# Kernel optimization log

Hardware: AMD Instinct MI355X
Metric: run time of the kernel (lower is better)

The kernel has to match this reference:

```python
import jax, jax.numpy as jnp
import numpy as np


def _logmvv(a, b, c, NT):
    """Log-space batched matrix-vector-vector product (SparseKernelHmmLm.logmvv).

    a: (N, T, C)     log potentials per sparse state
    b: (N, T, C, D)  log left features
    c: (N, T, C, D)  log right features
    Returns (N, T, D, D): out[n,t,i,j] = logsumexp_c(a[n,t,c] + b[n,t,c,i] + c[n,t,c,j])
    Tokens are flattened and zero-padded to NT rows, as in the original kernel.
    """
    N, T, C = a.shape
    D = b.shape[-1]
    nt = N * T
    pad = NT - nt
    af = jnp.concatenate([a.reshape(nt, C), jnp.zeros((pad, C), a.dtype)], 0)          # (NT, C)
    bf = jnp.concatenate([b.reshape(nt, C, D), jnp.zeros((pad, C, D), b.dtype)], 0)    # (NT, C, D)
    cf = jnp.concatenate([c.reshape(nt, C, D), jnp.zeros((pad, C, D), c.dtype)], 0)    # (NT, C, D)

    ab = af[:, :, None] + bf                      # (NT, C, D) log(a*b)
    m1 = jnp.max(ab, axis=1)                      # (NT, D) stabilizer for left factor
    m2 = jnp.max(cf, axis=1)                      # (NT, D) stabilizer for right factor
    e1 = jnp.exp(ab - m1[:, None, :])             # (NT, C, D)
    e2 = jnp.exp(cf - m2[:, None, :])             # (NT, C, D)
    # contraction over sparse states C -> (NT, D, D)
    s = jnp.einsum('nci,ncj->nij', e1, e2)
    out = jnp.log(s) + m1[:, :, None] + m2[:, None, :]
    return out[:nt].reshape(N, T, D, D)


def setup_inputs() -> dict:
    key = jax.random.key(0)
    k1, k2, k3 = jax.random.split(key, 3)
    N, T, C, D = 8, 250, 128, 64
    a = jax.random.normal(k1, (N, T, C), dtype=jnp.float32)
    b = jax.random.normal(k2, (N, T, C, D), dtype=jnp.float32)
    c = jax.random.normal(k3, (N, T, C, D), dtype=jnp.float32)
    return {"a": a, "b": b, "c": c, "NT": 2048}


def reference(a, b, c, NT):
    return _logmvv(a, b, c, NT)
```

## Files before the change

### kernel.cpp

```cpp
#include <hip/hip_runtime.h>
#include <stdint.h>

typedef __attribute__((ext_vector_type(8))) short short8;
typedef __attribute__((ext_vector_type(4))) float f32x4;

#define CDIM 128
#define DDIM 64

__device__ __forceinline__ uint32_t pack2_bf16(float a, float b) {
  uint32_t ua = __float_as_uint(a);
  uint32_t ub = __float_as_uint(b);
  ua = (ua + 0x7FFFu + ((ua >> 16) & 1u)) >> 16;
  ub = (ub + 0x7FFFu + ((ub >> 16) & 1u)) >> 16;
  return ua | (ub << 16);
}

__global__ __launch_bounds__(256, 8) void logmvv_kernel(
    const float* __restrict__ a, const float* __restrict__ b,
    const float* __restrict__ c, float* __restrict__ out) {
  __shared__ float a_lds[CDIM];
  __shared__ __align__(16) uint16_t e2T[DDIM * CDIM];

  const int row = blockIdx.x;
  const int t = threadIdx.x;
  const int lane = t & 63;
  const int w = t >> 6;
  const int l15 = lane & 15;
  const int lq = lane >> 4;
  const int swz = (lane & 7) << 4;

  const float* bp = b + (size_t)row * (CDIM * DDIM);
  const float* cp = c + (size_t)row * (CDIM * DDIM);

  if (t < CDIM) a_lds[t] = a[(size_t)row * CDIM + t];

  char* e2b = (char*)e2T;
#pragma unroll
  for (int k = 0; k < 4; ++k) {
    float cv[8];
#pragma unroll
    for (int p = 0; p < 8; ++p) cv[p] = cp[(w * 32 + k * 8 + p) * DDIM + lane];
    const uint32_t r0 = pack2_bf16(__expf(cv[0]), __expf(cv[1]));
    const uint32_t r1 = pack2_bf16(__expf(cv[2]), __expf(cv[3]));
    const uint32_t r2 = pack2_bf16(__expf(cv[4]), __expf(cv[5]));
    const uint32_t r3 = pack2_bf16(__expf(cv[6]), __expf(cv[7]));
    *(uint4*)(e2b + lane * 256 + ((w * 64 + k * 16) ^ swz)) =
        make_uint4(r0, r1, r2, r3);
  }

  __syncthreads();

  short8 afrag[4];
  const int colA = 16 * w + l15;
#pragma unroll
  for (int kk = 0; kk < 4; ++kk) {
    const int cbase = kk * 32 + lq * 8;
    float bv[8];
#pragma unroll
    for (int e = 0; e < 8; ++e)
      bv[e] = bp[(cbase + e) * DDIM + colA] + a_lds[cbase + e];
    union { uint32_t u[4]; short8 s; } fr;
    fr.u[0] = pack2_bf16(__expf(bv[0]), __expf(bv[1]));
    fr.u[1] = pack2_bf16(__expf(bv[2]), __expf(bv[3]));
    fr.u[2] = pack2_bf16(__expf(bv[4]), __expf(bv[5]));
    fr.u[3] = pack2_bf16(__expf(bv[6]), __expf(bv[7]));
    afrag[kk] = fr.s;
  }

  f32x4 acc[4];
#pragma unroll
  for (int tj = 0; tj < 4; ++tj) acc[tj] = (f32x4){0.f, 0.f, 0.f, 0.f};

#pragma unroll
  for (int kk = 0; kk < 4; ++kk) {
    const int cb = kk * 64 + lq * 16;
#pragma unroll
    for (int tj = 0; tj < 4; ++tj) {
      const short8 bf =
          *(const short8*)(e2b + (16 * tj + l15) * 256 + (cb ^ swz));
      acc[tj] =
          __builtin_amdgcn_mfma_f32_16x16x32_bf16(afrag[kk], bf, acc[tj], 0, 0, 0);
    }
  }

  float* op = out + (size_t)row * (DDIM * DDIM);
#pragma unroll
  for (int tj = 0; tj < 4; ++tj) {
#pragma unroll
    for (int rr = 0; rr < 4; ++rr) {
      op[(16 * w + lq * 4 + rr) * DDIM + 16 * tj + l15] = __logf(acc[tj][rr]);
    }
  }
}

extern "C" void kernel_launch(void* const* d_in, const int* in_sizes, int n_in,
                              void* d_out, int out_size, void* d_ws, size_t ws_size,
                              hipStream_t stream) {
  const float* a = (const float*)d_in[0];
  const float* b = (const float*)d_in[1];
  const float* c = (const float*)d_in[2];
  float* out = (float*)d_out;
  const int nt = in_sizes[0] / CDIM;
  logmvv_kernel<<<nt, 256, 0, stream>>>(a, b, c, out);
}
```

Before: 29.26 us.

## Use one wave per row with register fragments, dropping the LDS transpose

Switches from four waves per token row, which staged exp(c) through swizzled LDS, to a single 64-lane wave per row. That wave loads both b and c fragments straight from global memory into registers and computes the full 64x64 output with a 4x4 grid of MFMA accumulators. This removes the LDS staging, the barrier and the shared a buffer. In exchange each wave needs far more registers (64 accumulator floats plus 64 loaded values per step), has less parallelism per row, and makes strided 16-wide global loads.

```diff
diff --git a/kernel.cpp b/kernel.cpp
--- a/kernel.cpp
+++ b/kernel.cpp
@@ -15,82 +15,80 @@
   return ua | (ub << 16);
 }
 
-__global__ __launch_bounds__(256, 8) void logmvv_kernel(
+__global__ __launch_bounds__(64, 2) void logmvv_kernel(
     const float* __restrict__ a, const float* __restrict__ b,
     const float* __restrict__ c, float* __restrict__ out) {
-  __shared__ float a_lds[CDIM];
-  __shared__ __align__(16) uint16_t e2T[DDIM * CDIM];
-
   const int row = blockIdx.x;
-  const int t = threadIdx.x;
-  const int lane = t & 63;
-  const int w = t >> 6;
+  const int lane = threadIdx.x;
   const int l15 = lane & 15;
   const int lq = lane >> 4;
-  const int swz = (lane & 7) << 4;
 
+  const float* ap = a + (size_t)row * CDIM;
   const float* bp = b + (size_t)row * (CDIM * DDIM);
   const float* cp = c + (size_t)row * (CDIM * DDIM);
 
-  if (t < CDIM) a_lds[t] = a[(size_t)row * CDIM + t];
+  f32x4 acc[4][4];
+#pragma unroll
+  for (int tr = 0; tr < 4; ++tr)
+#pragma unroll
+    for (int tj = 0; tj < 4; ++tj) acc[tr][tj] = (f32x4){0.f, 0.f, 0.f, 0.f};
 
-  char* e2b = (char*)e2T;
-#pragma unroll
-  for (int k = 0; k < 4; ++k) {
-    float cv[8];
-#pragma unroll
-    for (int p = 0; p < 8; ++p) cv[p] = cp[(w * 32 + k * 8 + p) * DDIM + lane];
-    const uint32_t r0 = pack2_bf16(__expf(cv[0]), __expf(cv[1]));
-    const uint32_t r1 = pack2_bf16(__expf(cv[2]), __expf(cv[3]));
-    const uint32_t r2 = pack2_bf16(__expf(cv[4]), __expf(cv[5]));
-    const uint32_t r3 = pack2_bf16(__expf(cv[6]), __expf(cv[7]));
-    *(uint4*)(e2b + lane * 256 + ((w * 64 + k * 16) ^ swz)) =
-        make_uint4(r0, r1, r2, r3);
-  }
-
-  __syncthreads();
-
-  short8 afrag[4];
-  const int colA = 16 * w + l15;
 #pragma unroll
   for (int kk = 0; kk < 4; ++kk) {
     const int cbase = kk * 32 + lq * 8;
-    float bv[8];
+
+    const float4 a0 = *(const float4*)(ap + cbase);
+    const float4 a1 = *(const float4*)(ap + cbase + 4);
+    float bv[4][8], cv[4][8];
 #pragma unroll
-    for (int e = 0; e < 8; ++e)
-      bv[e] = bp[(cbase + e) * DDIM + colA] + a_lds[cbase + e];
-    union { uint32_t u[4]; short8 s; } fr;
-    fr.u[0] = pack2_bf16(__expf(bv[0]), __expf(bv[1]));
-    fr.u[1] = pack2_bf16(__expf(bv[2]), __expf(bv[3]));
-    fr.u[2] = pack2_bf16(__expf(bv[4]), __expf(bv[5]));
-    fr.u[3] = pack2_bf16(__expf(bv[6]), __expf(bv[7]));
-    afrag[kk] = fr.s;
-  }
+    for (int tr = 0; tr < 4; ++tr)
+#pragma unroll
+      for (int e = 0; e < 8; ++e)
+        bv[tr][e] = bp[(cbase + e) * DDIM + 16 * tr + l15];
+#pragma unroll
+    for (int tj = 0; tj < 4; ++tj)
+#pragma unroll
+      for (int e = 0; e < 8; ++e)
+        cv[tj][e] = cp[(cbase + e) * DDIM + 16 * tj + l15];
 
-  f32x4 acc[4];
+    const float av[8] = {a0.x, a0.y, a0.z, a0.w, a1.x, a1.y, a1.z, a1.w};
+
+    short8 afrag[4], bfrag[4];
 #pragma unroll
-  for (int tj = 0; tj < 4; ++tj) acc[tj] = (f32x4){0.f, 0.f, 0.f, 0.f};
+    for (int tr = 0; tr < 4; ++tr) {
+      union { uint32_t u[4]; short8 s; } fr;
+#pragma unroll
+      for (int p = 0; p < 4; ++p)
+        fr.u[p] = pack2_bf16(__expf(av[2 * p] + bv[tr][2 * p]),
+                             __expf(av[2 * p + 1] + bv[tr][2 * p + 1]));
+      afrag[tr] = fr.s;
+    }
+#pragma unroll
+    for (int tj = 0; tj < 4; ++tj) {
+      union { uint32_t u[4]; short8 s; } fr;
+#pragma unroll
+      for (int p = 0; p < 4; ++p)
+        fr.u[p] = pack2_bf16(__expf(cv[tj][2 * p]), __expf(cv[tj][2 * p + 1]));
+      bfrag[tj] = fr.s;
+    }
 
 #pragma unroll
-  for (int kk = 0; kk < 4; ++kk) {
-    const int cb = kk * 64 + lq * 16;
+    for (int tr = 0; tr < 4; ++tr)
 #pragma unroll
-    for (int tj = 0; tj < 4; ++tj) {
-      const short8 bf =
-          *(const short8*)(e2b + (16 * tj + l15) * 256 + (cb ^ swz));
-      acc[tj] =
-          __builtin_amdgcn_mfma_f32_16x16x32_bf16(afrag[kk], bf, acc[tj], 0, 0, 0);
-    }
+      for (int tj = 0; tj < 4; ++tj)
+        acc[tr][tj] = __builtin_amdgcn_mfma_f32_16x16x32_bf16(
+            afrag[tr], bfrag[tj], acc[tr][tj], 0, 0, 0);
   }
 
   float* op = out + (size_t)row * (DDIM * DDIM);
 #pragma unroll
-  for (int tj = 0; tj < 4; ++tj) {
+  for (int tr = 0; tr < 4; ++tr)
 #pragma unroll
-    for (int rr = 0; rr < 4; ++rr) {
-      op[(16 * w + lq * 4 + rr) * DDIM + 16 * tj + l15] = __logf(acc[tj][rr]);
-    }
-  }
+    for (int tj = 0; tj < 4; ++tj)
+#pragma unroll
+      for (int rr = 0; rr < 4; ++rr)
+        op[(16 * tr + lq * 4 + rr) * DDIM + 16 * tj + l15] =
+            __logf(acc[tr][tj][rr]);
 }
 
 extern "C" void kernel_launch(void* const* d_in, const int* in_sizes, int n_in,
@@ -101,5 +99,5 @@
   const float* c = (const float*)d_in[2];
   float* out = (float*)d_out;
   const int nt = in_sizes[0] / CDIM;
-  logmvv_kernel<<<nt, 256, 0, stream>>>(a, b, c, out);
+  logmvv_kernel<<<nt, 64, 0, stream>>>(a, b, c, out);
 }
```

New measurement: 37.27 us. 1.27x slower.

## Issue all global loads up front and drop the a LDS staging

Applied to the files above, without the earlier changes.

All of c, b and a are now loaded into registers at kernel start, so the memory requests overlap instead of being issued in dependent batches. The a vector is read straight from global with float4 loads rather than staged through shared memory. The A-fragment exp/pack work is moved before the barrier so it overlaps the LDS writes of other waves. The extra live registers mean launch bounds drop from 8 to 4 blocks per SIMD hint, which may reduce occupancy.

```diff
diff --git a/kernel.cpp b/kernel.cpp
--- a/kernel.cpp
+++ b/kernel.cpp
@@ -15,10 +15,9 @@
   return ua | (ub << 16);
 }
 
-__global__ __launch_bounds__(256, 8) void logmvv_kernel(
+__global__ __launch_bounds__(256, 4) void logmvv_kernel(
     const float* __restrict__ a, const float* __restrict__ b,
     const float* __restrict__ c, float* __restrict__ out) {
-  __shared__ float a_lds[CDIM];
   __shared__ __align__(16) uint16_t e2T[DDIM * CDIM];
 
   const int row = blockIdx.x;
@@ -29,43 +28,54 @@
   const int lq = lane >> 4;
   const int swz = (lane & 7) << 4;
 
+  const float* ap = a + (size_t)row * CDIM;
   const float* bp = b + (size_t)row * (CDIM * DDIM);
   const float* cp = c + (size_t)row * (CDIM * DDIM);
 
-  if (t < CDIM) a_lds[t] = a[(size_t)row * CDIM + t];
+  float cv[32];
+#pragma unroll
+  for (int p = 0; p < 32; ++p) cv[p] = cp[(w * 32 + p) * DDIM + lane];
+
+  const int colA = 16 * w + l15;
+  float bvv[4][8];
+#pragma unroll
+  for (int kk = 0; kk < 4; ++kk)
+#pragma unroll
+    for (int e = 0; e < 8; ++e)
+      bvv[kk][e] = bp[(kk * 32 + lq * 8 + e) * DDIM + colA];
+  float av[4][8];
+#pragma unroll
+  for (int kk = 0; kk < 4; ++kk) {
+    const float4 a0 = *(const float4*)(ap + kk * 32 + lq * 8);
+    const float4 a1 = *(const float4*)(ap + kk * 32 + lq * 8 + 4);
+    av[kk][0] = a0.x; av[kk][1] = a0.y; av[kk][2] = a0.z; av[kk][3] = a0.w;
+    av[kk][4] = a1.x; av[kk][5] = a1.y; av[kk][6] = a1.z; av[kk][7] = a1.w;
+  }
 
   char* e2b = (char*)e2T;
 #pragma unroll
   for (int k = 0; k < 4; ++k) {
-    float cv[8];
-#pragma unroll
-    for (int p = 0; p < 8; ++p) cv[p] = cp[(w * 32 + k * 8 + p) * DDIM + lane];
-    const uint32_t r0 = pack2_bf16(__expf(cv[0]), __expf(cv[1]));
-    const uint32_t r1 = pack2_bf16(__expf(cv[2]), __expf(cv[3]));
-    const uint32_t r2 = pack2_bf16(__expf(cv[4]), __expf(cv[5]));
-    const uint32_t r3 = pack2_bf16(__expf(cv[6]), __expf(cv[7]));
+    const uint32_t r0 = pack2_bf16(__expf(cv[k * 8 + 0]), __expf(cv[k * 8 + 1]));
+    const uint32_t r1 = pack2_bf16(__expf(cv[k * 8 + 2]), __expf(cv[k * 8 + 3]));
+    const uint32_t r2 = pack2_bf16(__expf(cv[k * 8 + 4]), __expf(cv[k * 8 + 5]));
+    const uint32_t r3 = pack2_bf16(__expf(cv[k * 8 + 6]), __expf(cv[k * 8 + 7]));
     *(uint4*)(e2b + lane * 256 + ((w * 64 + k * 16) ^ swz)) =
         make_uint4(r0, r1, r2, r3);
   }
 
-  __syncthreads();
-
   short8 afrag[4];
-  const int colA = 16 * w + l15;
 #pragma unroll
   for (int kk = 0; kk < 4; ++kk) {
-    const int cbase = kk * 32 + lq * 8;
-    float bv[8];
+    union { uint32_t u[4]; short8 s; } fr;
 #pragma unroll
-    for (int e = 0; e < 8; ++e)
-      bv[e] = bp[(cbase + e) * DDIM + colA] + a_lds[cbase + e];
-    union { uint32_t u[4]; short8 s; } fr;
-    fr.u[0] = pack2_bf16(__expf(bv[0]), __expf(bv[1]));
-    fr.u[1] = pack2_bf16(__expf(bv[2]), __expf(bv[3]));
-    fr.u[2] = pack2_bf16(__expf(bv[4]), __expf(bv[5]));
-    fr.u[3] = pack2_bf16(__expf(bv[6]), __expf(bv[7]));
+    for (int p = 0; p < 4; ++p)
+      fr.u[p] = pack2_bf16(__expf(av[kk][2 * p] + bvv[kk][2 * p]),
+                           __expf(av[kk][2 * p + 1] + bvv[kk][2 * p + 1]));
     afrag[kk] = fr.s;
   }
+  asm volatile("" ::"v"(afrag[0]), "v"(afrag[1]), "v"(afrag[2]), "v"(afrag[3]));
+
+  __syncthreads();
 
   f32x4 acc[4];
 #pragma unroll
@@ -85,12 +95,10 @@
 
   float* op = out + (size_t)row * (DDIM * DDIM);
 #pragma unroll
-  for (int tj = 0; tj < 4; ++tj) {
+  for (int tj = 0; tj < 4; ++tj)
 #pragma unroll
-    for (int rr = 0; rr < 4; ++rr) {
+    for (int rr = 0; rr < 4; ++rr)
       op[(16 * w + lq * 4 + rr) * DDIM + 16 * tj + l15] = __logf(acc[tj][rr]);
-    }
-  }
 }
 
 extern "C" void kernel_launch(void* const* d_in, const int* in_sizes, int n_in,
```

Measured after the change: 29.28 us. About the same (+0.1%).

## Process eight rows per block with double-buffered async global-to-LDS staging

Applied to the files above, without the earlier changes.

Each block now handles eight token rows in sequence instead of one. The b and c tiles for the next row are prefetched with global_load_lds into a second LDS buffer while the current row is exponentiated and multiplied, with hand-placed vmcnt waits and barriers between the stages. The aim is to hide global memory latency behind compute and to cut per-block launch overhead. The cost is about 148 KB of LDS per block, which allows one block (four waves) per CU and sharply lowers occupancy and memory-level parallelism for this bandwidth-bound kernel.

```diff
diff --git a/kernel.cpp b/kernel.cpp
--- a/kernel.cpp
+++ b/kernel.cpp
@@ -6,6 +6,7 @@
 
 #define CDIM 128
 #define DDIM 64
+#define RPB 8
 
 __device__ __forceinline__ uint32_t pack2_bf16(float a, float b) {
   uint32_t ua = __float_as_uint(a);
@@ -15,82 +16,130 @@
   return ua | (ub << 16);
 }
 
-__global__ __launch_bounds__(256, 8) void logmvv_kernel(
+__global__ __launch_bounds__(256, 1) void logmvv_kernel(
     const float* __restrict__ a, const float* __restrict__ b,
-    const float* __restrict__ c, float* __restrict__ out) {
-  __shared__ float a_lds[CDIM];
+    const float* __restrict__ c, float* __restrict__ out, int nt) {
+  __shared__ __align__(16) float bRaw[2][CDIM * DDIM];
+  __shared__ __align__(16) float cRaw[2][CDIM * DDIM];
   __shared__ __align__(16) uint16_t e2T[DDIM * CDIM];
+  __shared__ __align__(16) float aLds[RPB * CDIM];
 
-  const int row = blockIdx.x;
   const int t = threadIdx.x;
   const int lane = t & 63;
   const int w = t >> 6;
   const int l15 = lane & 15;
   const int lq = lane >> 4;
   const int swz = (lane & 7) << 4;
+  const int bid = blockIdx.x;
+  const int row0 = bid * RPB;
+  const int rows = (nt - row0 < RPB) ? (nt - row0) : RPB;
 
-  const float* bp = b + (size_t)row * (CDIM * DDIM);
-  const float* cp = c + (size_t)row * (CDIM * DDIM);
+  __builtin_amdgcn_global_load_lds(
+      (const __attribute__((address_space(1))) void*)(a + (size_t)row0 * CDIM +
+                                                      w * 256 + lane * 4),
+      (__attribute__((address_space(3))) void*)((char*)aLds + w * 1024), 16, 0, 0);
 
-  if (t < CDIM) a_lds[t] = a[(size_t)row * CDIM + t];
-
-  char* e2b = (char*)e2T;
-#pragma unroll
-  for (int k = 0; k < 4; ++k) {
-    float cv[8];
-#pragma unroll
-    for (int p = 0; p < 8; ++p) cv[p] = cp[(w * 32 + k * 8 + p) * DDIM + lane];
-    const uint32_t r0 = pack2_bf16(__expf(cv[0]), __expf(cv[1]));
-    const uint32_t r1 = pack2_bf16(__expf(cv[2]), __expf(cv[3]));
-    const uint32_t r2 = pack2_bf16(__expf(cv[4]), __expf(cv[5]));
-    const uint32_t r3 = pack2_bf16(__expf(cv[6]), __expf(cv[7]));
-    *(uint4*)(e2b + lane * 256 + ((w * 64 + k * 16) ^ swz)) =
-        make_uint4(r0, r1, r2, r3);
+#define STAGE(ridx, buf)                                                        \
+  {                                                                             \
+    const float* bsrc = b + (size_t)(ridx) * (CDIM * DDIM);                     \
+    const float* csrc = c + (size_t)(ridx) * (CDIM * DDIM);                     \
+    _Pragma("unroll") for (int q = 0; q < 8; ++q) {                             \
+      const int chunk = w * 8 + q;                            \
+      __builtin_amdgcn_global_load_lds(                                         \
+          (const __attribute__((address_space(1))) void*)(bsrc + chunk * 256 +  \
+                                                          lane * 4),            \
+          (__attribute__((address_space(3))) void*)((char*)bRaw[buf] +          \
+                                                    chunk * 1024),              \
+          16, 0, 0);                                                            \
+      __builtin_amdgcn_global_load_lds(                                         \
+          (const __attribute__((address_space(1))) void*)(csrc + chunk * 256 +  \
+                                                          lane * 4),            \
+          (__attribute__((address_space(3))) void*)((char*)cRaw[buf] +          \
+                                                    chunk * 1024),              \
+          16, 0, 0);                                                            \
+    }                                                                           \
   }
 
-  __syncthreads();
+  STAGE(row0, 0);
 
-  short8 afrag[4];
+  int cur = 0;
   const int colA = 16 * w + l15;
+  char* e2b = (char*)e2T;
+
+  for (int i = 0; i < rows; ++i) {
+    const int row = row0 + i;
+    const bool have_next = (i + 1 < rows);
+    if (have_next) STAGE(row + 1, cur ^ 1);
+
+    if (i == 0 && !have_next) {
+      asm volatile("s_waitcnt vmcnt(0)" ::: "memory");
+    } else if (i == 0 || !have_next) {
+      asm volatile("s_waitcnt vmcnt(16)" ::: "memory");
+    } else {
+      asm volatile("s_waitcnt vmcnt(32)" ::: "memory");
+    }
+    __builtin_amdgcn_s_barrier();
+    __builtin_amdgcn_sched_barrier(0);
+
+    const float* cr = cRaw[cur];
 #pragma unroll
-  for (int kk = 0; kk < 4; ++kk) {
-    const int cbase = kk * 32 + lq * 8;
-    float bv[8];
+    for (int k = 0; k < 4; ++k) {
+      float cvv[8];
 #pragma unroll
-    for (int e = 0; e < 8; ++e)
-      bv[e] = bp[(cbase + e) * DDIM + colA] + a_lds[cbase + e];
-    union { uint32_t u[4]; short8 s; } fr;
-    fr.u[0] = pack2_bf16(__expf(bv[0]), __expf(bv[1]));
-    fr.u[1] = pack2_bf16(__expf(bv[2]), __expf(bv[3]));
-    fr.u[2] = pack2_bf16(__expf(bv[4]), __expf(bv[5]));
-    fr.u[3] = pack2_bf16(__expf(bv[6]), __expf(bv[7]));
-    afrag[kk] = fr.s;
+      for (int p = 0; p < 8; ++p) cvv[p] = cr[(w * 32 + k * 8 + p) * DDIM + lane];
+      const uint32_t r0 = pack2_bf16(__expf(cvv[0]), __expf(cvv[1]));
+      const uint32_t r1 = pack2_bf16(__expf(cvv[2]), __expf(cvv[3]));
+      const uint32_t r2 = pack2_bf16(__expf(cvv[4]), __expf(cvv[5]));
+      const uint32_t r3 = pack2_bf16(__expf(cvv[6]), __expf(cvv[7]));
+      *(uint4*)(e2b + lane * 256 + ((w * 64 + k * 16) ^ swz)) =
+          make_uint4(r0, r1, r2, r3);
+    }
+
+    const float* br = bRaw[cur];
+    short8 afrag[4];
+#pragma unroll
+    for (int kk = 0; kk < 4; ++kk) {
+      const int cbase = kk * 32 + lq * 8;
+      float bv[8];
+#pragma unroll
+      for (int e = 0; e < 8; ++e)
+        bv[e] = br[(cbase + e) * DDIM + colA] + aLds[i * CDIM + cbase + e];
+      union { uint32_t u[4]; short8 s; } fr;
+#pragma unroll
+      for (int p = 0; p < 4; ++p)
+        fr.u[p] = pack2_bf16(__expf(bv[2 * p]), __expf(bv[2 * p + 1]));
+      afrag[kk] = fr.s;
+    }
+
+    asm volatile("s_waitcnt lgkmcnt(0)" ::: "memory");
+    __builtin_amdgcn_s_barrier();
+    __builtin_amdgcn_sched_barrier(0);
+
+    f32x4 acc[4];
+#pragma unroll
+    for (int tj = 0; tj < 4; ++tj) acc[tj] = (f32x4){0.f, 0.f, 0.f, 0.f};
+#pragma unroll
+    for (int kk = 0; kk < 4; ++kk) {
+      const int cb = kk * 64 + lq * 16;
+#pragma unroll
+      for (int tj = 0; tj < 4; ++tj) {
+        const short8 bf =
+            *(const short8*)(e2b + (16 * tj + l15) * 256 + (cb ^ swz));
+        acc[tj] = __builtin_amdgcn_mfma_f32_16x16x32_bf16(afrag[kk], bf,
+                                                          acc[tj], 0, 0, 0);
+      }
+    }
+
+    float* op = out + (size_t)row * (DDIM * DDIM);
+#pragma unroll
+    for (int tj = 0; tj < 4; ++tj)
+#pragma unroll
+      for (int rr = 0; rr < 4; ++rr)
+        op[(16 * w + lq * 4 + rr) * DDIM + 16 * tj + l15] = __logf(acc[tj][rr]);
+
+    cur ^= 1;
   }
-
-  f32x4 acc[4];
-#pragma unroll
-  for (int tj = 0; tj < 4; ++tj) acc[tj] = (f32x4){0.f, 0.f, 0.f, 0.f};
-
-#pragma unroll
-  for (int kk = 0; kk < 4; ++kk) {
-    const int cb = kk * 64 + lq * 16;
-#pragma unroll
-    for (int tj = 0; tj < 4; ++tj) {
-      const short8 bf =
-          *(const short8*)(e2b + (16 * tj + l15) * 256 + (cb ^ swz));
-      acc[tj] =
-          __builtin_amdgcn_mfma_f32_16x16x32_bf16(afrag[kk], bf, acc[tj], 0, 0, 0);
-    }
-  }
-
-  float* op = out + (size_t)row * (DDIM * DDIM);
-#pragma unroll
-  for (int tj = 0; tj < 4; ++tj) {
-#pragma unroll
-    for (int rr = 0; rr < 4; ++rr) {
-      op[(16 * w + lq * 4 + rr) * DDIM + 16 * tj + l15] = __logf(acc[tj][rr]);
-    }
-  }
+#undef STAGE
 }
 
 extern "C" void kernel_launch(void* const* d_in, const int* in_sizes, int n_in,
@@ -101,5 +150,6 @@
   const float* c = (const float*)d_in[2];
   float* out = (float*)d_out;
   const int nt = in_sizes[0] / CDIM;
-  logmvv_kernel<<<nt, 256, 0, stream>>>(a, b, c, out);
+  const int grid = (nt + RPB - 1) / RPB;
+  logmvv_kernel<<<grid, 256, 0, stream>>>(a, b, c, out, nt);
 }
```

Result: slower. 40.70 us (+39.1%).
